# Optimization experiments

Hardware: AMD Instinct MI355X
Metric: run time of the kernel (lower is better)

## Reference

```python
import jax, jax.numpy as jnp
import numpy as np

# module config (matches init_kwargs)
NUM_CHIPS = 8
EPC = 8                 # experts_per_chip
E = 64                  # n_routed_experts = NUM_CHIPS * EPC
K = 4                   # num_experts_per_tok
META = 8                # metadata_len
M = 1024                # max_dispatched_tokens_per_expert
S = 512                 # seq_len_per_chip
H = 2048                # hidden_dim


def setup_inputs() -> dict:
    key = jax.random.key(0)
    k1, k2, k3 = jax.random.split(key, 3)
    x = jax.random.normal(k1, (NUM_CHIPS, S, H), jnp.float32)
    weights = jax.random.normal(k2, (NUM_CHIPS, S, K), jnp.float32)
    indices = jax.random.randint(k3, (NUM_CHIPS, S, K), 0, E, dtype=jnp.int32)
    return {"x": x, "weights": weights, "indices": indices}


def _local_ranks(f):
    # f: (S*K,) expert ids for one chip, in loop order (token-major, topk-minor).
    # rank[i] = number of earlier entries routed to the same expert.
    oh = (f[:, None] == jnp.arange(E)[None, :]).astype(jnp.int32)  # (SK, E)
    csum = jnp.cumsum(oh, axis=0)
    return jnp.take_along_axis(csum, f[:, None], axis=1)[:, 0] - 1


def reference(x, weights, indices):
    C, S_, K_ = indices.shape
    f = indices.reshape(C, S_ * K_)  # (C, SK) routed expert per dispatch entry

    # per-(chip, expert) token counts, then exclusive prefix-sum over chips -> base offsets
    counts = jax.vmap(lambda fi: jnp.zeros((E,), jnp.int32).at[fi].add(1))(f)  # (C, E)
    cum = jnp.cumsum(counts, axis=0)
    offset_base = jnp.concatenate([jnp.zeros((1, E), jnp.int32), cum[:-1]], axis=0)
    tokens_per_expert = cum[-1].reshape(NUM_CHIPS, EPC).astype(jnp.int32)

    # destination slot within each expert buffer = base offset + within-chip arrival rank
    rank = jax.vmap(_local_ranks)(f)                                 # (C, SK)
    dst = jnp.take_along_axis(offset_base, f, axis=1) + rank         # (C, SK)
    # expert_chip*EPC + expert_within_chip == routed_expert, so flat buffer row = f*M + dst
    slot = (f * M + dst).reshape(-1)                                 # (C*SK,)

    # scatter token hidden states
    x_entries = jnp.broadcast_to(x[:, :, None, :], (C, S_, K_, H)).reshape(-1, H)
    dispatched = (jnp.zeros((E * M, H), jnp.float32)
                  .at[slot].set(x_entries)
                  .reshape(NUM_CHIPS, EPC, M, H))

    # scatter metadata rows [chip, token, topk_idx, expert, int(weight), 0...]
    chip_ids = jnp.broadcast_to(jnp.arange(C)[:, None, None], (C, S_, K_)).reshape(-1)
    tok_ids = jnp.broadcast_to(jnp.arange(S_)[None, :, None], (C, S_, K_)).reshape(-1)
    k_ids = jnp.broadcast_to(jnp.arange(K_)[None, None, :], (C, S_, K_)).reshape(-1)
    w_int = weights.reshape(-1).astype(jnp.int32)  # original writes float into int32 buffer (truncates)
    meta_rows = jnp.stack([chip_ids, tok_ids, k_ids, f.reshape(-1), w_int], axis=1).astype(jnp.int32)
    meta_rows = jnp.concatenate(
        [meta_rows, jnp.zeros((meta_rows.shape[0], META - 5), jnp.int32)], axis=1)
    metadata = (jnp.full((E * M, META), -1, jnp.int32)
                .at[slot].set(meta_rows)
                .reshape(NUM_CHIPS, EPC, M, META))

    return dispatched, metadata, tokens_per_expert
```

## Files before the change

kernel.cpp:

```cpp
#include <hip/hip_runtime.h>

#define NUM_CHIPS 8
#define EPC 8
#define E_EXPERTS 64
#define TOPK 4
#define META 8
#define M_CAP 1024
#define SEQ 512
#define HID 2048
#define SK (SEQ * TOPK)
#define ROWS (E_EXPERTS * M_CAP)

#define DISP_SZ ((size_t)ROWS * HID)
#define META_OFF DISP_SZ
#define TOK_OFF (DISP_SZ + (size_t)ROWS * META)

#define WS_INV 0
#define WS_CNT (ROWS)
#define WS_OFB (ROWS + 512)
#define WS_TOT (ROWS + 1024)

typedef float vfloat4 __attribute__((ext_vector_type(4)));

__global__ __launch_bounds__(256) void count_kernel(const int* __restrict__ idx,
                                                    int* __restrict__ ws) {
    const int c = blockIdx.x;
    const int t = threadIdx.x;
    __shared__ __align__(16) unsigned char f[SK];
    __shared__ int partial[4][E_EXPERTS];

    const int* ic = idx + c * SK;
    for (int i = t; i < SK; i += 256) f[i] = (unsigned char)ic[i];
    __syncthreads();

    const int e = t & 63;
    const int q = t >> 6;
    const unsigned eb = (unsigned)e;
    const unsigned* fw = (const unsigned*)f;
    int cnt = 0;
    for (int w = q * 128; w < q * 128 + 128; ++w) {
        unsigned v = fw[w];
        cnt += ((v & 0xffu) == eb);
        cnt += (((v >> 8) & 0xffu) == eb);
        cnt += (((v >> 16) & 0xffu) == eb);
        cnt += ((v >> 24) == eb);
    }
    partial[q][e] = cnt;
    __syncthreads();
    if (q == 0) {
        int s = partial[0][e] + partial[1][e] + partial[2][e] + partial[3][e];
        ws[WS_CNT + c * E_EXPERTS + e] = s;
    }
}

__global__ void prefix_kernel(int* __restrict__ ws, float* __restrict__ out) {
    const int e = threadIdx.x;
    int base = 0;
    for (int c = 0; c < NUM_CHIPS; ++c) {
        ws[WS_OFB + c * E_EXPERTS + e] = base;
        base += ws[WS_CNT + c * E_EXPERTS + e];
    }
    ws[WS_TOT + e] = base;
    out[TOK_OFF + e] = (float)base;
}

__global__ __launch_bounds__(256) void rank_kernel(const int* __restrict__ idx,
                                                   int* __restrict__ ws) {
    const int c = blockIdx.x;
    const int t = threadIdx.x;
    __shared__ __align__(16) unsigned char f[SK];
    __shared__ int partial[4][E_EXPERTS];

    const int* ic = idx + c * SK;
    for (int i = t; i < SK; i += 256) f[i] = (unsigned char)ic[i];
    __syncthreads();

    const int e = t & 63;
    const int q = t >> 6;
    const unsigned eb = (unsigned)e;
    const unsigned* fw = (const unsigned*)f;
    int cnt = 0;
    for (int w = q * 128; w < q * 128 + 128; ++w) {
        unsigned v = fw[w];
        cnt += ((v & 0xffu) == eb);
        cnt += (((v >> 8) & 0xffu) == eb);
        cnt += (((v >> 16) & 0xffu) == eb);
        cnt += ((v >> 24) == eb);
    }
    partial[q][e] = cnt;
    __syncthreads();

    int base = ws[WS_OFB + c * E_EXPERTS + e];
    for (int qq = 0; qq < q; ++qq) base += partial[qq][e];

    int* inv = ws + WS_INV;
    for (int i = q * 512; i < q * 512 + 512; ++i) {
        if ((int)f[i] == e) {
            inv[e * M_CAP + base] = c * SK + i;
            ++base;
        }
    }
}

#define RPB 16
#define FILL_GRID (ROWS / RPB)

__global__ __launch_bounds__(256) void fill_kernel(const float* __restrict__ x,
                                                   const float* __restrict__ wts,
                                                   const int* __restrict__ ws,
                                                   float* __restrict__ out) {
    const int t = threadIdx.x;
    const int base_row = blockIdx.x * RPB;
    const int e = base_row >> 10;
    const int p0 = base_row & (M_CAP - 1);

    const int total = ws[WS_TOT + e];
    int nused = total - p0;
    if (nused < 0) nused = 0;
    if (nused > RPB) nused = RPB;

    if (nused > 0) {
        int entry = ws[WS_INV + base_row];
        const vfloat4* s4 = (const vfloat4*)(x + (size_t)(entry >> 2) * HID);
        vfloat4 v0 = s4[t];
        vfloat4 v1 = s4[t + 256];

        for (int r = 0; r < nused; ++r) {
            const int cur = entry;
            vfloat4 w0 = v0;
            vfloat4 w1 = v1;
            if (r + 1 < nused) {
                entry = ws[WS_INV + base_row + r + 1];
                const vfloat4* n4 = (const vfloat4*)(x + (size_t)(entry >> 2) * HID);
                v0 = n4[t];
                v1 = n4[t + 256];
            }
            vfloat4* d4 = (vfloat4*)(out + (size_t)(base_row + r) * HID);
            d4[t] = w0;
            d4[t + 256] = w1;

            if (t < META) {
                float mv;
                if (t == 0)      mv = (float)(cur >> 11);
                else if (t == 1) mv = (float)((cur >> 2) & (SEQ - 1));
                else if (t == 2) mv = (float)(cur & 3);
                else if (t == 3) mv = (float)e;
                else if (t == 4) mv = (float)((int)wts[cur]);
                else             mv = 0.0f;
                out[META_OFF + (size_t)(base_row + r) * META + t] = mv;
            }
        }
    }

    const vfloat4 z = (vfloat4)(0.0f);
    for (int r = nused; r < RPB; ++r) {
        vfloat4* d4 = (vfloat4*)(out + (size_t)(base_row + r) * HID);
        d4[t] = z;
        d4[t + 256] = z;
        if (t < META) out[META_OFF + (size_t)(base_row + r) * META + t] = -1.0f;
    }
}

extern "C" void kernel_launch(void* const* d_in, const int* in_sizes, int n_in,
                              void* d_out, int out_size, void* d_ws, size_t ws_size,
                              hipStream_t stream) {
    const float* x   = (const float*)d_in[0];
    const float* wts = (const float*)d_in[1];
    const int* idx   = (const int*)d_in[2];
    float* out = (float*)d_out;
    int* ws = (int*)d_ws;

    count_kernel<<<NUM_CHIPS, 256, 0, stream>>>(idx, ws);
    prefix_kernel<<<1, 64, 0, stream>>>(ws, out);
    rank_kernel<<<NUM_CHIPS, 256, 0, stream>>>(idx, ws);
    fill_kernel<<<FILL_GRID, 256, 0, stream>>>(x, wts, ws, out);
}
```

Measured before the change: 628.4 us.

## Split dispatch fill into compact gather copy, tail zeroing, and metadata kernels

Builds a compacted list of used (entry, destination row) pairs during ranking. A dedicated kernel then copies only used rows with 8 unrolled independent row loads per block. Zeroing of unused rows and metadata writing move into separate kernels. This removes the serial per-block row loop and the load imbalance of the old fill kernel, at the cost of two extra launches and extra workspace writes.

```diff
diff --git a/kernel.cpp b/kernel.cpp
--- a/kernel.cpp
+++ b/kernel.cpp
@@ -9,6 +9,7 @@
 #define SEQ 512
 #define HID 2048
 #define SK (SEQ * TOPK)
+#define NENT (NUM_CHIPS * SK)
 #define ROWS (E_EXPERTS * M_CAP)
 
 #define DISP_SZ ((size_t)ROWS * HID)
@@ -16,9 +17,12 @@
 #define TOK_OFF (DISP_SZ + (size_t)ROWS * META)
 
 #define WS_INV 0
-#define WS_CNT (ROWS)
-#define WS_OFB (ROWS + 512)
-#define WS_TOT (ROWS + 1024)
+#define WS_CNT 65536
+#define WS_OFB 66048
+#define WS_TOT 66560
+#define WS_GB 66624
+#define WS_DENT 66688
+#define WS_DROW 83072
 
 typedef float vfloat4 __attribute__((ext_vector_type(4)));
 
@@ -62,6 +66,14 @@
     }
     ws[WS_TOT + e] = base;
     out[TOK_OFF + e] = (float)base;
+
+    __shared__ int tot[E_EXPERTS];
+    tot[e] = base;
+    __syncthreads();
+    if (e == 0) {
+        int g = 0;
+        for (int i = 0; i < E_EXPERTS; ++i) { ws[WS_GB + i] = g; g += tot[i]; }
+    }
 }
 
 __global__ __launch_bounds__(256) void rank_kernel(const int* __restrict__ idx,
@@ -92,72 +104,87 @@
 
     int base = ws[WS_OFB + c * E_EXPERTS + e];
     for (int qq = 0; qq < q; ++qq) base += partial[qq][e];
-
-    int* inv = ws + WS_INV;
+    const int gb = ws[WS_GB + e];
+
     for (int i = q * 512; i < q * 512 + 512; ++i) {
         if ((int)f[i] == e) {
-            inv[e * M_CAP + base] = c * SK + i;
+            const int entry = c * SK + i;
+            ws[WS_INV + e * M_CAP + base] = entry;
+            ws[WS_DENT + gb + base] = entry;
+            ws[WS_DROW + gb + base] = e * M_CAP + base;
             ++base;
         }
     }
 }
 
-#define RPB 16
-#define FILL_GRID (ROWS / RPB)
-
-__global__ __launch_bounds__(256) void fill_kernel(const float* __restrict__ x,
-                                                   const float* __restrict__ wts,
-                                                   const int* __restrict__ ws,
-                                                   float* __restrict__ out) {
-    const int t = threadIdx.x;
-    const int base_row = blockIdx.x * RPB;
+#define ZRPB 16
+#define ZERO_GRID (ROWS / ZRPB)
+
+__global__ __launch_bounds__(256) void zero_tail(const int* __restrict__ ws,
+                                                 float* __restrict__ out) {
+    const int t = threadIdx.x;
+    const int base_row = blockIdx.x * ZRPB;
     const int e = base_row >> 10;
     const int p0 = base_row & (M_CAP - 1);
 
     const int total = ws[WS_TOT + e];
     int nused = total - p0;
     if (nused < 0) nused = 0;
-    if (nused > RPB) nused = RPB;
-
-    if (nused > 0) {
-        int entry = ws[WS_INV + base_row];
-        const vfloat4* s4 = (const vfloat4*)(x + (size_t)(entry >> 2) * HID);
-        vfloat4 v0 = s4[t];
-        vfloat4 v1 = s4[t + 256];
-
-        for (int r = 0; r < nused; ++r) {
-            const int cur = entry;
-            vfloat4 w0 = v0;
-            vfloat4 w1 = v1;
-            if (r + 1 < nused) {
-                entry = ws[WS_INV + base_row + r + 1];
-                const vfloat4* n4 = (const vfloat4*)(x + (size_t)(entry >> 2) * HID);
-                v0 = n4[t];
-                v1 = n4[t + 256];
-            }
-            vfloat4* d4 = (vfloat4*)(out + (size_t)(base_row + r) * HID);
-            d4[t] = w0;
-            d4[t + 256] = w1;
-
-            if (t < META) {
-                float mv;
-                if (t == 0)      mv = (float)(cur >> 11);
-                else if (t == 1) mv = (float)((cur >> 2) & (SEQ - 1));
-                else if (t == 2) mv = (float)(cur & 3);
-                else if (t == 3) mv = (float)e;
-                else if (t == 4) mv = (float)((int)wts[cur]);
-                else             mv = 0.0f;
-                out[META_OFF + (size_t)(base_row + r) * META + t] = mv;
-            }
-        }
-    }
+    if (nused > ZRPB) nused = ZRPB;
 
     const vfloat4 z = (vfloat4)(0.0f);
-    for (int r = nused; r < RPB; ++r) {
+    for (int r = nused; r < ZRPB; ++r) {
         vfloat4* d4 = (vfloat4*)(out + (size_t)(base_row + r) * HID);
         d4[t] = z;
         d4[t + 256] = z;
-        if (t < META) out[META_OFF + (size_t)(base_row + r) * META + t] = -1.0f;
+    }
+}
+
+__global__ __launch_bounds__(256) void meta_kernel(const float* __restrict__ wts,
+                                                   const int* __restrict__ ws,
+                                                   float* __restrict__ out) {
+    const int t = threadIdx.x;
+    const int row = blockIdx.x * 32 + (t >> 3);
+    const int j = t & 7;
+    const int e = row >> 10;
+    const int p = row & (M_CAP - 1);
+
+    float mv = -1.0f;
+    if (p < ws[WS_TOT + e]) {
+        const int entry = ws[WS_INV + row];
+        if (j == 0)      mv = (float)(entry >> 11);
+        else if (j == 1) mv = (float)((entry >> 2) & (SEQ - 1));
+        else if (j == 2) mv = (float)(entry & 3);
+        else if (j == 3) mv = (float)e;
+        else if (j == 4) mv = (float)((int)wts[entry]);
+        else             mv = 0.0f;
+    }
+    out[META_OFF + (size_t)row * META + j] = mv;
+}
+
+#define RPU 8
+#define USED_GRID (NENT / RPU)
+
+__global__ __launch_bounds__(256) void fill_used(const float* __restrict__ x,
+                                                 const int* __restrict__ ws,
+                                                 float* __restrict__ out) {
+    const int t = threadIdx.x;
+    const int g0 = blockIdx.x * RPU;
+
+    __shared__ int sh_ent[RPU];
+    __shared__ int sh_row[RPU];
+    if (t < RPU)           sh_ent[t] = ws[WS_DENT + g0 + t];
+    else if (t < 2 * RPU)  sh_row[t - RPU] = ws[WS_DROW + g0 + (t - RPU)];
+    __syncthreads();
+
+#pragma unroll
+    for (int r = 0; r < RPU; ++r) {
+        const vfloat4* s4 = (const vfloat4*)(x + (size_t)(sh_ent[r] >> 2) * HID);
+        vfloat4* d4 = (vfloat4*)(out + (size_t)sh_row[r] * HID);
+        vfloat4 v0 = s4[t];
+        vfloat4 v1 = s4[t + 256];
+        d4[t] = v0;
+        d4[t + 256] = v1;
     }
 }
 
@@ -173,5 +200,7 @@
     count_kernel<<<NUM_CHIPS, 256, 0, stream>>>(idx, ws);
     prefix_kernel<<<1, 64, 0, stream>>>(ws, out);
     rank_kernel<<<NUM_CHIPS, 256, 0, stream>>>(idx, ws);
-    fill_kernel<<<FILL_GRID, 256, 0, stream>>>(x, wts, ws, out);
-}
+    zero_tail<<<ZERO_GRID, 256, 0, stream>>>(ws, out);
+    meta_kernel<<<ROWS / 32, 256, 0, stream>>>(wts, ws, out);
+    fill_used<<<USED_GRID, 256, 0, stream>>>(x, ws, out);
+}
```

Measured after the change: 615.5 us. -2.0%, faster.
